# Kernel tuning notes

Measured on AMD Instinct MI355X. Metric: run time of the kernel, lower is better.

Reference implementation:

```python
import jax, jax.numpy as jnp
import numpy as np

L, N, E, H = 2048, 2, 1024, 16
D = E // H  # head dim = 64


def setup_inputs() -> dict:
    key = jax.random.key(0)
    k1, k2, k3, k4, k5 = jax.random.split(key, 5)
    s = 1.0 / np.sqrt(E)
    return {
        "x": jax.random.normal(k1, (L, N, E), dtype=jnp.float32),
        "in_proj_weight": jax.random.normal(k2, (3 * E, E), dtype=jnp.float32) * s,
        "in_proj_bias": jax.random.normal(k3, (3 * E,), dtype=jnp.float32) * 0.01,
        "out_proj_weight": jax.random.normal(k4, (E, E), dtype=jnp.float32) * s,
        "out_proj_bias": jax.random.normal(k5, (E,), dtype=jnp.float32) * 0.01,
    }


def reference(x, in_proj_weight, in_proj_bias, out_proj_weight, out_proj_bias):
    # packed qkv in-projection: (L, N, 3E)
    qkv = jnp.einsum("lne,fe->lnf", x, in_proj_weight) + in_proj_bias
    q, k, v = jnp.split(qkv, 3, axis=-1)

    def heads(t):  # (L, N, E) -> (N, H, L, D)
        return t.reshape(L, N, H, D).transpose(1, 2, 0, 3)

    q, k, v = heads(q), heads(k), heads(v)
    scale = 1.0 / jnp.sqrt(jnp.asarray(D, dtype=q.dtype))
    scores = jnp.einsum("nhld,nhmd->nhlm", q * scale, k)  # (N, H, L, L)
    attn = jax.nn.softmax(scores, axis=-1)
    out = jnp.einsum("nhlm,nhmd->nhld", attn, v)  # (N, H, L, D)
    out = out.transpose(2, 0, 1, 3).reshape(L, N, E)
    return jnp.einsum("lne,fe->lnf", out, out_proj_weight) + out_proj_bias
```

## Files before the change

### kernel.cpp

```cpp
#include <hip/hip_runtime.h>

typedef __attribute__((ext_vector_type(8))) short bf16x8;
typedef __attribute__((ext_vector_type(4))) float f32x4;
typedef __attribute__((ext_vector_type(16))) float f32x16;
typedef __attribute__((ext_vector_type(8))) unsigned short ushort8;
typedef __attribute__((ext_vector_type(4))) unsigned short ushort4_t;
typedef __attribute__((ext_vector_type(4))) unsigned uint4_t;

#define LSEQ 2048
#define NB 2
#define EMB 1024
#define NHEAD 16
#define HD 64

__device__ __forceinline__ unsigned short f2bf(float f) {
  unsigned u = __builtin_bit_cast(unsigned, f);
  u += 0x7fffu + ((u >> 16) & 1u);
  return (unsigned short)(u >> 16);
}
__device__ __forceinline__ float bf2f(unsigned short s) {
  return __builtin_bit_cast(float, ((unsigned)s) << 16);
}

__device__ __forceinline__ void gll16(const void* g, void* l) {
  __builtin_amdgcn_global_load_lds((const __attribute__((address_space(1))) unsigned*)g,
                                   (__attribute__((address_space(3))) unsigned*)l, 16, 0, 0);
}

__global__ __launch_bounds__(256) void cvt_all(const float* __restrict__ x,
                                               const float* __restrict__ wq,
                                               const float* __restrict__ wo,
                                               unsigned short* __restrict__ xb,
                                               unsigned short* __restrict__ wqb,
                                               unsigned short* __restrict__ wob) {
  int i = blockIdx.x * 256 + threadIdx.x;
  const float* src;
  unsigned short* dst;
  int off;
  if (i < 1048576) { src = x;  dst = xb;  off = i; }
  else if (i < 1835008) { src = wq; dst = wqb; off = i - 1048576; }
  else { src = wo; dst = wob; off = i - 1835008; }
  float4 v = ((const float4*)src)[off];
  ushort4_t o;
  o.x = f2bf(v.x); o.y = f2bf(v.y); o.z = f2bf(v.z); o.w = f2bf(v.w);
  ((ushort4_t*)dst)[off] = o;
}

template <bool OUT_BF16>
__global__ __launch_bounds__(256, 2) void gemm_bf16_nt(
    const unsigned short* __restrict__ A, const unsigned short* __restrict__ B,
    const float* __restrict__ bias, void* __restrict__ Cout, int M, int Ncol, int K) {
  __shared__ unsigned short Asm[2][128 * 64];
  __shared__ unsigned short Bsm[2][128 * 64];
  const int tid = threadIdx.x;
  const int wave = tid >> 6, lane = tid & 63;
  const int wr = (wave >> 1) * 64, wc = (wave & 1) * 64;
  const int lr = lane & 15, lg = lane >> 4;
  const int bm = blockIdx.x * 128, bn = blockIdx.y * 128;

  f32x4 acc[4][4];
#pragma unroll
  for (int i = 0; i < 4; ++i)
#pragma unroll
    for (int j = 0; j < 4; ++j) acc[i][j] = (f32x4){0.f, 0.f, 0.f, 0.f};

  auto stage = [&](int buf, int kt) {
#pragma unroll
    for (int c = 0; c < 4; ++c) {
      int idx = (c * 4 + wave) * 64 + lane;
      int row = idx >> 3, ch = (idx & 7) * 8;
      gll16(A + (size_t)(bm + row) * K + kt * 64 + ch, &Asm[buf][(c * 4 + wave) * 512]);
      gll16(B + (size_t)(bn + row) * K + kt * 64 + ch, &Bsm[buf][(c * 4 + wave) * 512]);
    }
  };

  const int nk = K >> 6;
  stage(0, 0);
  __syncthreads();
  int cur = 0;

  for (int kt = 0; kt < nk; ++kt) {
    if (kt < nk - 1) stage(cur ^ 1, kt + 1);
#pragma unroll
    for (int ks = 0; ks < 2; ++ks) {
      bf16x8 af[4], bfr[4];
#pragma unroll
      for (int i = 0; i < 4; ++i)
        af[i] = *(const bf16x8*)&Asm[cur][(wr + i * 16 + lr) * 64 + ks * 32 + lg * 8];
#pragma unroll
      for (int j = 0; j < 4; ++j)
        bfr[j] = *(const bf16x8*)&Bsm[cur][(wc + j * 16 + lr) * 64 + ks * 32 + lg * 8];
      __builtin_amdgcn_s_setprio(1);
#pragma unroll
      for (int i = 0; i < 4; ++i)
#pragma unroll
        for (int j = 0; j < 4; ++j)
          acc[i][j] = __builtin_amdgcn_mfma_f32_16x16x32_bf16(af[i], bfr[j], acc[i][j], 0, 0, 0);
      __builtin_amdgcn_s_setprio(0);
    }
    __syncthreads();
    cur ^= 1;
  }
#pragma unroll
  for (int i = 0; i < 4; ++i) {
#pragma unroll
    for (int j = 0; j < 4; ++j) {
      int col = bn + wc + j * 16 + lr;
      float bv = bias[col];
#pragma unroll
      for (int r = 0; r < 4; ++r) {
        int row = bm + wr + i * 16 + lg * 4 + r;
        float v = acc[i][j][r] + bv;
        if constexpr (OUT_BF16)
          ((unsigned short*)Cout)[(size_t)row * Ncol + col] = f2bf(v);
        else
          ((float*)Cout)[(size_t)row * Ncol + col] = v;
      }
    }
  }
}

__global__ __launch_bounds__(256) void transpose_v(const unsigned short* __restrict__ qkv,
                                                   unsigned short* __restrict__ vt) {
  __shared__ unsigned short t[64][72];
  const int nh = blockIdx.y, n = nh >> 4, h = nh & 15;
  const int lt = blockIdx.x * 64;
  const int tid = threadIdx.x;
#pragma unroll
  for (int it = 0; it < 2; ++it) {
    int idx = it * 256 + tid;
    int l = idx >> 3, ch = (idx & 7) * 8;
    ushort8 v = *(const ushort8*)(qkv + (size_t)((lt + l) * NB + n) * 3072 + 2 * EMB + h * HD + ch);
    *(ushort8*)&t[l][ch] = v;
  }
  __syncthreads();
  int d = tid >> 2, lc = (tid & 3) * 16;
  unsigned short tmp[16];
#pragma unroll
  for (int i = 0; i < 16; ++i) tmp[i] = t[lc + i][d];
#pragma unroll
  for (int i = 0; i < 2; ++i)
    *(ushort8*)(vt + (size_t)(nh * HD + d) * LSEQ + lt + lc + i * 8) = *(const ushort8*)&tmp[i * 8];
}

__global__ __launch_bounds__(256, 2) void flash_attn(const unsigned short* __restrict__ qkv,
                                                     const unsigned short* __restrict__ vt,
                                                     unsigned short* __restrict__ ob) {
  __shared__ unsigned short Ksm[2][128 * 64];
  __shared__ unsigned short Vsm[2][64 * 128];
  const int tid = threadIdx.x, wave = tid >> 6, lane = tid & 63;
  const int l31 = lane & 31, lh = lane >> 5;
  const int flat = blockIdx.y * 16 + blockIdx.x;
  const int fb = (flat & 7) * 64 + (flat >> 3);
  const int nh = fb >> 4, qt = fb & 15;
  const int n = nh >> 4, hh = nh & 15;
  const int q = qt * 128 + wave * 32 + l31;

  const int sch = ((lane & 7) ^ ((lane >> 3) & 7)) * 8;
  const unsigned short* Kbase = qkv + (size_t)n * 3072 + EMB + hh * HD + sch;
  const size_t vbase = (size_t)nh * HD * LSEQ;

  bf16x8 qf[4];
  {
    const unsigned short* qb = qkv + ((size_t)q * NB + n) * 3072 + hh * HD + lh * 8;
#pragma unroll
    for (int t = 0; t < 4; ++t) {
      bf16x8 tv = *(const bf16x8*)(qb + t * 16);
#pragma unroll
      for (int e = 0; e < 8; ++e)
        tv[e] = (short)f2bf(bf2f((unsigned short)tv[e]) * 0.18033688f);
      qf[t] = tv;
    }
  }

  auto stage = [&](int buf, int kt) {
#pragma unroll
    for (int c = 0; c < 4; ++c) {
      int cc = c * 4 + wave;
      int krow = cc * 8 + (lane >> 3);
      gll16(Kbase + (size_t)(kt * 128 + krow) * (NB * 3072), &Ksm[buf][cc * 512]);
      int vrow = cc * 4 + (lane >> 4);
      int schv = ((lane & 15) ^ ((cc & 1) * 4 + (lane >> 4))) * 8;
      gll16(vt + vbase + (size_t)vrow * LSEQ + kt * 128 + schv, &Vsm[buf][cc * 512]);
    }
  };

  float lsum = 0.f;
  f32x16 o0, o1;
#pragma unroll
  for (int r = 0; r < 16; ++r) { o0[r] = 0.f; o1[r] = 0.f; }

  stage(0, 0);
  __syncthreads();
  int cur = 0;
  const int swz = l31 & 7;

  for (int kt = 0; kt < LSEQ / 128; ++kt) {
    if (kt < LSEQ / 128 - 1) stage(cur ^ 1, kt + 1);

    f32x16 s[4];
#pragma unroll
    for (int kb = 0; kb < 4; ++kb)
#pragma unroll
      for (int r = 0; r < 16; ++r) s[kb][r] = 0.f;
    __builtin_amdgcn_s_setprio(1);
#pragma unroll
    for (int t = 0; t < 4; ++t) {
      int ch = ((t * 2 + lh) ^ swz) * 8;
#pragma unroll
      for (int kb = 0; kb < 4; ++kb) {
        bf16x8 kf = *(const bf16x8*)&Ksm[cur][(kb * 32 + l31) * 64 + ch];
        s[kb] = __builtin_amdgcn_mfma_f32_32x32x16_bf16(kf, qf[t], s[kb], 0, 0, 0);
      }
    }
    __builtin_amdgcn_s_setprio(0);

    float ps0 = 0.f, ps1 = 0.f, ps2 = 0.f, ps3 = 0.f;
#pragma unroll
    for (int kb = 0; kb < 4; ++kb) {
#pragma unroll
      for (int r = 0; r < 16; r += 4) {
        float p0 = exp2f(s[kb][r]);
        float p1 = exp2f(s[kb][r + 1]);
        float p2 = exp2f(s[kb][r + 2]);
        float p3 = exp2f(s[kb][r + 3]);
        s[kb][r] = p0; s[kb][r + 1] = p1; s[kb][r + 2] = p2; s[kb][r + 3] = p3;
        ps0 += p0; ps1 += p1; ps2 += p2; ps3 += p3;
      }
    }
    lsum += (ps0 + ps1) + (ps2 + ps3);

    bf16x8 pf[8];
#pragma unroll
    for (int half = 0; half < 2; ++half) {
      const f32x16& sa = s[half * 2];
      const f32x16& sb = s[half * 2 + 1];
#pragma unroll
      for (int g = 0; g < 4; ++g) {
        const int b = (g & 1) * 8;
        float a0 = (g < 2) ? sa[b + 0] : sb[b + 0];
        float a1 = (g < 2) ? sa[b + 1] : sb[b + 1];
        float a2 = (g < 2) ? sa[b + 2] : sb[b + 2];
        float a3 = (g < 2) ? sa[b + 3] : sb[b + 3];
        float a4 = (g < 2) ? sa[b + 4] : sb[b + 4];
        float a5 = (g < 2) ? sa[b + 5] : sb[b + 5];
        float a6 = (g < 2) ? sa[b + 6] : sb[b + 6];
        float a7 = (g < 2) ? sa[b + 7] : sb[b + 7];
        unsigned w0, w1, w2, w3;
        asm("v_cvt_pk_bf16_f32 %0, %1, %2" : "=v"(w0) : "v"(a0), "v"(a1));
        asm("v_cvt_pk_bf16_f32 %0, %1, %2" : "=v"(w1) : "v"(a2), "v"(a3));
        asm("v_cvt_pk_bf16_f32 %0, %1, %2" : "=v"(w2) : "v"(a4), "v"(a5));
        asm("v_cvt_pk_bf16_f32 %0, %1, %2" : "=v"(w3) : "v"(a6), "v"(a7));
        asm("v_permlane32_swap_b32 %0, %1" : "+v"(w0), "+v"(w2));
        asm("v_permlane32_swap_b32 %0, %1" : "+v"(w1), "+v"(w3));
        pf[half * 4 + g] = __builtin_bit_cast(bf16x8, (uint4_t){w0, w1, w2, w3});
      }
    }

    __builtin_amdgcn_s_setprio(1);
#pragma unroll
    for (int u = 0; u < 8; ++u) {
      int ch = ((u * 2 + lh) ^ swz) * 8;
      bf16x8 a0 = *(const bf16x8*)&Vsm[cur][l31 * 128 + ch];
      bf16x8 a1 = *(const bf16x8*)&Vsm[cur][(32 + l31) * 128 + ch];
      o0 = __builtin_amdgcn_mfma_f32_32x32x16_bf16(a0, pf[u], o0, 0, 0, 0);
      o1 = __builtin_amdgcn_mfma_f32_32x32x16_bf16(a1, pf[u], o1, 0, 0, 0);
    }
    __builtin_amdgcn_s_setprio(0);

    __syncthreads();
    cur ^= 1;
  }

  lsum += __shfl_xor(lsum, 32);
  float inv = 1.0f / lsum;
  unsigned short* op = ob + ((size_t)q * NB + n) * EMB + hh * HD;
#pragma unroll
  for (int g = 0; g < 4; ++g) {
    ushort4_t pk0, pk1;
#pragma unroll
    for (int e = 0; e < 4; ++e) {
      pk0[e] = f2bf(o0[g * 4 + e] * inv);
      pk1[e] = f2bf(o1[g * 4 + e] * inv);
    }
    *(ushort4_t*)(op + g * 8 + lh * 4) = pk0;
    *(ushort4_t*)(op + 32 + g * 8 + lh * 4) = pk1;
  }
}

extern "C" void kernel_launch(void* const* d_in, const int* in_sizes, int n_in,
                              void* d_out, int out_size, void* d_ws, size_t ws_size,
                              hipStream_t stream) {
  const float* x = (const float*)d_in[0];
  const float* wqkv = (const float*)d_in[1];
  const float* bqkv = (const float*)d_in[2];
  const float* wout = (const float*)d_in[3];
  const float* bout = (const float*)d_in[4];

  char* ws = (char*)d_ws;
  unsigned short* xb    = (unsigned short*)(ws);
  unsigned short* wqkvb = (unsigned short*)(ws + 8388608);
  unsigned short* woutb = (unsigned short*)(ws + 14680064);
  unsigned short* qkvb  = (unsigned short*)(ws + 16777216);
  unsigned short* vtb   = (unsigned short*)(ws + 41943040);
  unsigned short* obuf  = (unsigned short*)(ws + 50331648);

  cvt_all<<<8192, 256, 0, stream>>>(x, wqkv, wout, xb, wqkvb, woutb);

  dim3 g1(32, 24);
  gemm_bf16_nt<true><<<g1, 256, 0, stream>>>(xb, wqkvb, bqkv, qkvb, 4096, 3072, 1024);

  dim3 gt(32, 32);
  transpose_v<<<gt, 256, 0, stream>>>(qkvb, vtb);

  dim3 g2(16, 32);
  flash_attn<<<g2, 256, 0, stream>>>(qkvb, vtb, obuf);

  dim3 g3(32, 8);
  gemm_bf16_nt<false><<<g3, 256, 0, stream>>>(obuf, woutb, bout, d_out, 4096, 1024, 1024);
}
```

Measured before the change: 215.1 us.

## Split attention over key halves with fp32 partials and a combine kernel

The flash attention kernel now splits each query tile's keys into two halves, doubling the block count to 1024. Each block uses 64-key tiles with smaller LDS buffers and a higher occupancy target. Unnormalized fp32 partial outputs and row sums go to workspace, and a new combine kernel adds the halves, normalizes and converts to bf16. This buys more parallelism and occupancy at the cost of extra global traffic (two fp32 partial buffers) and one more kernel launch. It relies on no running max, so adding the two halves' sums directly is valid, as in the original code.

```diff
diff --git a/kernel.cpp b/kernel.cpp
--- a/kernel.cpp
+++ b/kernel.cpp
@@ -143,22 +143,25 @@
     *(ushort8*)(vt + (size_t)(nh * HD + d) * LSEQ + lt + lc + i * 8) = *(const ushort8*)&tmp[i * 8];
 }
 
-__global__ __launch_bounds__(256, 2) void flash_attn(const unsigned short* __restrict__ qkv,
+__global__ __launch_bounds__(256, 4) void flash_attn(const unsigned short* __restrict__ qkv,
                                                      const unsigned short* __restrict__ vt,
-                                                     unsigned short* __restrict__ ob) {
-  __shared__ unsigned short Ksm[2][128 * 64];
-  __shared__ unsigned short Vsm[2][64 * 128];
+                                                     float* __restrict__ Op,
+                                                     float* __restrict__ Lp) {
+  __shared__ unsigned short Ksm[2][64 * 64];
+  __shared__ unsigned short Vsm[2][64 * 64];
   const int tid = threadIdx.x, wave = tid >> 6, lane = tid & 63;
   const int l31 = lane & 31, lh = lane >> 5;
-  const int flat = blockIdx.y * 16 + blockIdx.x;
-  const int fb = (flat & 7) * 64 + (flat >> 3);
-  const int nh = fb >> 4, qt = fb & 15;
+  const int flat = blockIdx.x;
+  const int fb = (flat & 7) * 128 + (flat >> 3);
+  const int nh = fb >> 5, rem = fb & 31;
+  const int qt = rem >> 1, half = rem & 1;
   const int n = nh >> 4, hh = nh & 15;
   const int q = qt * 128 + wave * 32 + l31;
+  const int key0 = half * (LSEQ / 2);
 
   const int sch = ((lane & 7) ^ ((lane >> 3) & 7)) * 8;
   const unsigned short* Kbase = qkv + (size_t)n * 3072 + EMB + hh * HD + sch;
-  const size_t vbase = (size_t)nh * HD * LSEQ;
+  const unsigned short* Vbase = vt + (size_t)nh * HD * LSEQ + sch;
 
   bf16x8 qf[4];
   {
@@ -175,13 +178,10 @@
 
   auto stage = [&](int buf, int kt) {
 #pragma unroll
-    for (int c = 0; c < 4; ++c) {
-      int cc = c * 4 + wave;
-      int krow = cc * 8 + (lane >> 3);
-      gll16(Kbase + (size_t)(kt * 128 + krow) * (NB * 3072), &Ksm[buf][cc * 512]);
-      int vrow = cc * 4 + (lane >> 4);
-      int schv = ((lane & 15) ^ ((cc & 1) * 4 + (lane >> 4))) * 8;
-      gll16(vt + vbase + (size_t)vrow * LSEQ + kt * 128 + schv, &Vsm[buf][cc * 512]);
+    for (int c = 0; c < 2; ++c) {
+      int row = ((c * 4 + wave) * 64 + lane) >> 3;
+      gll16(Kbase + (size_t)(key0 + kt * 64 + row) * (NB * 3072), &Ksm[buf][(c * 4 + wave) * 512]);
+      gll16(Vbase + (size_t)row * LSEQ + key0 + kt * 64, &Vsm[buf][(c * 4 + wave) * 512]);
     }
   };
 
@@ -194,75 +194,66 @@
   __syncthreads();
   int cur = 0;
   const int swz = l31 & 7;
-
-  for (int kt = 0; kt < LSEQ / 128; ++kt) {
-    if (kt < LSEQ / 128 - 1) stage(cur ^ 1, kt + 1);
-
-    f32x16 s[4];
-#pragma unroll
-    for (int kb = 0; kb < 4; ++kb)
-#pragma unroll
-      for (int r = 0; r < 16; ++r) s[kb][r] = 0.f;
+  const int NT = (LSEQ / 2) / 64;
+
+  for (int kt = 0; kt < NT; ++kt) {
+    if (kt < NT - 1) stage(cur ^ 1, kt + 1);
+
+    f32x16 s0, s1;
+#pragma unroll
+    for (int r = 0; r < 16; ++r) { s0[r] = 0.f; s1[r] = 0.f; }
     __builtin_amdgcn_s_setprio(1);
 #pragma unroll
     for (int t = 0; t < 4; ++t) {
       int ch = ((t * 2 + lh) ^ swz) * 8;
-#pragma unroll
-      for (int kb = 0; kb < 4; ++kb) {
-        bf16x8 kf = *(const bf16x8*)&Ksm[cur][(kb * 32 + l31) * 64 + ch];
-        s[kb] = __builtin_amdgcn_mfma_f32_32x32x16_bf16(kf, qf[t], s[kb], 0, 0, 0);
-      }
+      bf16x8 k0 = *(const bf16x8*)&Ksm[cur][l31 * 64 + ch];
+      bf16x8 k1 = *(const bf16x8*)&Ksm[cur][(32 + l31) * 64 + ch];
+      s0 = __builtin_amdgcn_mfma_f32_32x32x16_bf16(k0, qf[t], s0, 0, 0, 0);
+      s1 = __builtin_amdgcn_mfma_f32_32x32x16_bf16(k1, qf[t], s1, 0, 0, 0);
     }
     __builtin_amdgcn_s_setprio(0);
 
     float ps0 = 0.f, ps1 = 0.f, ps2 = 0.f, ps3 = 0.f;
 #pragma unroll
-    for (int kb = 0; kb < 4; ++kb) {
-#pragma unroll
-      for (int r = 0; r < 16; r += 4) {
-        float p0 = exp2f(s[kb][r]);
-        float p1 = exp2f(s[kb][r + 1]);
-        float p2 = exp2f(s[kb][r + 2]);
-        float p3 = exp2f(s[kb][r + 3]);
-        s[kb][r] = p0; s[kb][r + 1] = p1; s[kb][r + 2] = p2; s[kb][r + 3] = p3;
-        ps0 += p0; ps1 += p1; ps2 += p2; ps3 += p3;
-      }
+    for (int r = 0; r < 16; r += 4) {
+      float a0 = exp2f(s0[r]),     b0 = exp2f(s1[r]);
+      float a1 = exp2f(s0[r + 1]), b1 = exp2f(s1[r + 1]);
+      float a2 = exp2f(s0[r + 2]), b2 = exp2f(s1[r + 2]);
+      float a3 = exp2f(s0[r + 3]), b3 = exp2f(s1[r + 3]);
+      s0[r] = a0; s0[r + 1] = a1; s0[r + 2] = a2; s0[r + 3] = a3;
+      s1[r] = b0; s1[r + 1] = b1; s1[r + 2] = b2; s1[r + 3] = b3;
+      ps0 += a0 + b0; ps1 += a1 + b1; ps2 += a2 + b2; ps3 += a3 + b3;
     }
     lsum += (ps0 + ps1) + (ps2 + ps3);
 
-    bf16x8 pf[8];
-#pragma unroll
-    for (int half = 0; half < 2; ++half) {
-      const f32x16& sa = s[half * 2];
-      const f32x16& sb = s[half * 2 + 1];
-#pragma unroll
-      for (int g = 0; g < 4; ++g) {
-        const int b = (g & 1) * 8;
-        float a0 = (g < 2) ? sa[b + 0] : sb[b + 0];
-        float a1 = (g < 2) ? sa[b + 1] : sb[b + 1];
-        float a2 = (g < 2) ? sa[b + 2] : sb[b + 2];
-        float a3 = (g < 2) ? sa[b + 3] : sb[b + 3];
-        float a4 = (g < 2) ? sa[b + 4] : sb[b + 4];
-        float a5 = (g < 2) ? sa[b + 5] : sb[b + 5];
-        float a6 = (g < 2) ? sa[b + 6] : sb[b + 6];
-        float a7 = (g < 2) ? sa[b + 7] : sb[b + 7];
-        unsigned w0, w1, w2, w3;
-        asm("v_cvt_pk_bf16_f32 %0, %1, %2" : "=v"(w0) : "v"(a0), "v"(a1));
-        asm("v_cvt_pk_bf16_f32 %0, %1, %2" : "=v"(w1) : "v"(a2), "v"(a3));
-        asm("v_cvt_pk_bf16_f32 %0, %1, %2" : "=v"(w2) : "v"(a4), "v"(a5));
-        asm("v_cvt_pk_bf16_f32 %0, %1, %2" : "=v"(w3) : "v"(a6), "v"(a7));
-        asm("v_permlane32_swap_b32 %0, %1" : "+v"(w0), "+v"(w2));
-        asm("v_permlane32_swap_b32 %0, %1" : "+v"(w1), "+v"(w3));
-        pf[half * 4 + g] = __builtin_bit_cast(bf16x8, (uint4_t){w0, w1, w2, w3});
-      }
+    bf16x8 pf[4];
+#pragma unroll
+    for (int g = 0; g < 4; ++g) {
+      const int b = (g & 1) * 8;
+      float a0 = (g < 2) ? s0[b + 0] : s1[b + 0];
+      float a1 = (g < 2) ? s0[b + 1] : s1[b + 1];
+      float a2 = (g < 2) ? s0[b + 2] : s1[b + 2];
+      float a3 = (g < 2) ? s0[b + 3] : s1[b + 3];
+      float a4 = (g < 2) ? s0[b + 4] : s1[b + 4];
+      float a5 = (g < 2) ? s0[b + 5] : s1[b + 5];
+      float a6 = (g < 2) ? s0[b + 6] : s1[b + 6];
+      float a7 = (g < 2) ? s0[b + 7] : s1[b + 7];
+      unsigned w0, w1, w2, w3;
+      asm("v_cvt_pk_bf16_f32 %0, %1, %2" : "=v"(w0) : "v"(a0), "v"(a1));
+      asm("v_cvt_pk_bf16_f32 %0, %1, %2" : "=v"(w1) : "v"(a2), "v"(a3));
+      asm("v_cvt_pk_bf16_f32 %0, %1, %2" : "=v"(w2) : "v"(a4), "v"(a5));
+      asm("v_cvt_pk_bf16_f32 %0, %1, %2" : "=v"(w3) : "v"(a6), "v"(a7));
+      asm("v_permlane32_swap_b32 %0, %1" : "+v"(w0), "+v"(w2));
+      asm("v_permlane32_swap_b32 %0, %1" : "+v"(w1), "+v"(w3));
+      pf[g] = __builtin_bit_cast(bf16x8, (uint4_t){w0, w1, w2, w3});
     }
 
     __builtin_amdgcn_s_setprio(1);
 #pragma unroll
-    for (int u = 0; u < 8; ++u) {
+    for (int u = 0; u < 4; ++u) {
       int ch = ((u * 2 + lh) ^ swz) * 8;
-      bf16x8 a0 = *(const bf16x8*)&Vsm[cur][l31 * 128 + ch];
-      bf16x8 a1 = *(const bf16x8*)&Vsm[cur][(32 + l31) * 128 + ch];
+      bf16x8 a0 = *(const bf16x8*)&Vsm[cur][l31 * 64 + ch];
+      bf16x8 a1 = *(const bf16x8*)&Vsm[cur][(32 + l31) * 64 + ch];
       o0 = __builtin_amdgcn_mfma_f32_32x32x16_bf16(a0, pf[u], o0, 0, 0, 0);
       o1 = __builtin_amdgcn_mfma_f32_32x32x16_bf16(a1, pf[u], o1, 0, 0, 0);
     }
@@ -272,20 +263,36 @@
     cur ^= 1;
   }
 
+  float* op = Op + (size_t)half * (4096 * 1024) + ((size_t)q * NB + n) * EMB + hh * HD;
+#pragma unroll
+  for (int g = 0; g < 4; ++g) {
+    float4 pk0, pk1;
+    pk0.x = o0[g * 4 + 0]; pk0.y = o0[g * 4 + 1]; pk0.z = o0[g * 4 + 2]; pk0.w = o0[g * 4 + 3];
+    pk1.x = o1[g * 4 + 0]; pk1.y = o1[g * 4 + 1]; pk1.z = o1[g * 4 + 2]; pk1.w = o1[g * 4 + 3];
+    *(float4*)(op + g * 8 + lh * 4) = pk0;
+    *(float4*)(op + 32 + g * 8 + lh * 4) = pk1;
+  }
   lsum += __shfl_xor(lsum, 32);
-  float inv = 1.0f / lsum;
-  unsigned short* op = ob + ((size_t)q * NB + n) * EMB + hh * HD;
-#pragma unroll
-  for (int g = 0; g < 4; ++g) {
-    ushort4_t pk0, pk1;
-#pragma unroll
-    for (int e = 0; e < 4; ++e) {
-      pk0[e] = f2bf(o0[g * 4 + e] * inv);
-      pk1[e] = f2bf(o1[g * 4 + e] * inv);
-    }
-    *(ushort4_t*)(op + g * 8 + lh * 4) = pk0;
-    *(ushort4_t*)(op + 32 + g * 8 + lh * 4) = pk1;
-  }
+  if (lh == 0)
+    Lp[(size_t)half * 65536 + ((size_t)q * NB + n) * NHEAD + hh] = lsum;
+}
+
+__global__ __launch_bounds__(256) void combine_o(const float* __restrict__ Op,
+                                                 const float* __restrict__ Lp,
+                                                 unsigned short* __restrict__ ob) {
+  int i = blockIdx.x * 256 + threadIdx.x;
+  float4 a = ((const float4*)Op)[i];
+  float4 b = ((const float4*)(Op + 4096 * 1024))[i];
+  int e = i << 2;
+  int qn = e >> 10, h = (e >> 6) & 15;
+  float l = Lp[qn * NHEAD + h] + Lp[65536 + qn * NHEAD + h];
+  float inv = 1.0f / l;
+  ushort4_t o;
+  o.x = f2bf((a.x + b.x) * inv);
+  o.y = f2bf((a.y + b.y) * inv);
+  o.z = f2bf((a.z + b.z) * inv);
+  o.w = f2bf((a.w + b.w) * inv);
+  ((ushort4_t*)ob)[i] = o;
 }
 
 extern "C" void kernel_launch(void* const* d_in, const int* in_sizes, int n_in,
@@ -304,6 +311,8 @@
   unsigned short* qkvb  = (unsigned short*)(ws + 16777216);
   unsigned short* vtb   = (unsigned short*)(ws + 41943040);
   unsigned short* obuf  = (unsigned short*)(ws + 50331648);
+  float*          Op    = (float*)(ws + 58720256);
+  float*          Lp    = (float*)(ws + 92274688);
 
   cvt_all<<<8192, 256, 0, stream>>>(x, wqkv, wout, xb, wqkvb, woutb);
 
@@ -313,8 +322,8 @@
   dim3 gt(32, 32);
   transpose_v<<<gt, 256, 0, stream>>>(qkvb, vtb);
 
-  dim3 g2(16, 32);
-  flash_attn<<<g2, 256, 0, stream>>>(qkvb, vtb, obuf);
+  flash_attn<<<1024, 256, 0, stream>>>(qkvb, vtb, Op, Lp);
+  combine_o<<<4096, 256, 0, stream>>>(Op, Lp, obuf);
 
   dim3 g3(32, 8);
   gemm_bf16_nt<false><<<g3, 256, 0, stream>>>(obuf, woutb, bout, d_out, 4096, 1024, 1024);
```

New measurement: 219.0 us. Within noise of the previous version (+1.8%).
